# Performance work log

Measured on AMD Instinct MI355X. Metric: run time of the kernel, lower is better.

## Reference

```python
import jax, jax.numpy as jnp
import numpy as np

EMBED = 1024
HEADS = 16
HEAD_DIM = EMBED // HEADS
N, L = 8, 1024


def setup_inputs() -> dict:
    key = jax.random.key(0)
    ks = jax.random.split(key, 12)
    s = 1.0 / np.sqrt(EMBED)
    return {
        "values": jax.random.normal(ks[0], (N, L, EMBED), jnp.float32),
        "keys": jax.random.normal(ks[1], (N, L, EMBED), jnp.float32),
        "queries": jax.random.normal(ks[2], (N, L, EMBED), jnp.float32),
        "mask": jax.random.randint(ks[3], (N, 1, L, L), 0, 2, jnp.int32),
        "Wv": jax.random.normal(ks[4], (EMBED, EMBED), jnp.float32) * s,
        "bv": jnp.zeros((EMBED,), jnp.float32),
        "Wk": jax.random.normal(ks[5], (EMBED, EMBED), jnp.float32) * s,
        "bk": jnp.zeros((EMBED,), jnp.float32),
        "Wq": jax.random.normal(ks[6], (EMBED, EMBED), jnp.float32) * s,
        "bq": jnp.zeros((EMBED,), jnp.float32),
        "Wo": jax.random.normal(ks[7], (EMBED, EMBED), jnp.float32) * s,
        "bo": jnp.zeros((EMBED,), jnp.float32),
    }


def reference(values, keys, queries, mask, Wv, bv, Wk, bk, Wq, bq, Wo, bo):
    n, q_len = queries.shape[0], queries.shape[1]
    # Linear projections (torch Linear: x @ W.T + b)
    v = values @ Wv.T + bv
    k = keys @ Wk.T + bk
    q = queries @ Wq.T + bq
    # split heads: [N, L, H, D]
    v = v.reshape(n, -1, HEADS, HEAD_DIM)
    k = k.reshape(n, -1, HEADS, HEAD_DIM)
    q = q.reshape(n, q_len, HEADS, HEAD_DIM)
    # energy: [N, H, Q, K]
    energy = jnp.einsum("nqhd,nkhd->nhqk", q, k)
    energy = jnp.where(mask == 0, jnp.float32(-1e20), energy)
    attention = jax.nn.softmax(energy / jnp.sqrt(jnp.float32(EMBED)), axis=3)
    out = jnp.einsum("nhqk,nkhd->nqhd", attention, v).reshape(n, q_len, EMBED)
    return out @ Wo.T + bo
```

## Files before the change

kernel.cpp:

```cpp
#include <hip/hip_runtime.h>
#include <hip/hip_bf16.h>


typedef __attribute__((ext_vector_type(8))) short short8;
typedef __attribute__((ext_vector_type(8))) __bf16 bf16x8;
typedef __attribute__((ext_vector_type(4))) float f32x4;
typedef __attribute__((ext_vector_type(16))) float f32x16;

static __device__ __forceinline__ unsigned short f2bf(float x) {
  union { float f; unsigned u; } v; v.f = x;
  unsigned r = v.u + 0x7FFFu + ((v.u >> 16) & 1u);
  return (unsigned short)(r >> 16);
}

static __device__ __forceinline__ f32x4 mfma16(short8 a, short8 b, f32x4 c) {
  return __builtin_amdgcn_mfma_f32_16x16x32_bf16(
      __builtin_bit_cast(bf16x8, a), __builtin_bit_cast(bf16x8, b), c, 0, 0, 0);
}
static __device__ __forceinline__ f32x16 mfma32(short8 a, short8 b, f32x16 c) {
  return __builtin_amdgcn_mfma_f32_32x32x16_bf16(
      __builtin_bit_cast(bf16x8, a), __builtin_bit_cast(bf16x8, b), c, 0, 0, 0);
}

static __device__ __forceinline__ void gll16(const unsigned short* g, unsigned short* l) {
  __builtin_amdgcn_global_load_lds(
      (const __attribute__((address_space(1))) unsigned int*)(const void*)g,
      (__attribute__((address_space(3))) unsigned int*)(void*)l, 16, 0, 0);
}

static __device__ __forceinline__ unsigned cvtpk(float lo, float hi) {
  unsigned r;
  asm("v_cvt_pk_bf16_f32 %0, %1, %2" : "=v"(r) : "v"(lo), "v"(hi));
  return r;
}

static __device__ __forceinline__ void cvt8(const float* __restrict__ in,
                                            unsigned short* __restrict__ out, int i) {
  float4 a = ((const float4*)in)[i * 2];
  float4 b = ((const float4*)in)[i * 2 + 1];
  union { short8 v; unsigned short u[8]; } pk;
  pk.u[0] = f2bf(a.x); pk.u[1] = f2bf(a.y); pk.u[2] = f2bf(a.z); pk.u[3] = f2bf(a.w);
  pk.u[4] = f2bf(b.x); pk.u[5] = f2bf(b.y); pk.u[6] = f2bf(b.z); pk.u[7] = f2bf(b.w);
  ((short8*)out)[i] = pk.v;
}

__global__ __launch_bounds__(256)
void fused_pre(const float* __restrict__ queries, const float* __restrict__ keys,
               const float* __restrict__ values,
               const float* __restrict__ Wq, const float* __restrict__ Wk,
               const float* __restrict__ Wv, const float* __restrict__ Wo,
               const int* __restrict__ mask,
               unsigned short* __restrict__ Xq, unsigned short* __restrict__ Xk,
               unsigned short* __restrict__ Xv,
               unsigned short* __restrict__ W4, unsigned long long* __restrict__ M64)
{
  const int bid = blockIdx.x, tid = threadIdx.x;
  if (bid < 4096) {
    cvt8(queries, Xq, bid * 256 + tid);
  } else if (bid < 8192) {
    cvt8(keys, Xk, (bid - 4096) * 256 + tid);
  } else if (bid < 10240) {
    const int wsel = (bid - 8192) >> 9;
    const float* src = wsel == 0 ? Wq : wsel == 1 ? Wk : wsel == 2 ? Wv : Wo;
    cvt8(src, W4 + wsel * 1048576, ((bid - 8192) & 511) * 256 + tid);
  } else if (bid < 11264) {
    const int lane = tid & 63, wid = tid >> 6;
    const int gw = (bid - 10240) * 4 + wid;
#pragma unroll 4
    for (int j = 0; j < 32; ++j) {
      const int w = gw * 32 + j;
      unsigned long long b = __ballot(mask[(size_t)w * 64 + lane] != 0);
      if (lane == 0) M64[w] = b;
    }
  } else {
    cvt8(values, Xv, (bid - 11264) * 256 + tid);
  }
}

template<int MODE>
__global__ __launch_bounds__(256)
void gemm_kernel(const unsigned short* __restrict__ A, const unsigned short* __restrict__ B,
                 const float* __restrict__ bias, void* __restrict__ outp, float oscale)
{
  __shared__ alignas(16) unsigned short As[128][32];
  __shared__ alignas(16) unsigned short Bs[128][32];
  const int tid = threadIdx.x, lane = tid & 63, wid = tid >> 6;
  const int l15 = lane & 15, lg = lane >> 4;
  const int j = blockIdx.x >> 3;
  int bm, bn;
  if (MODE == 3) { bn = (blockIdx.x & 7) * 8 + (j & 7); bm = j >> 3; }
  else           { bm = (blockIdx.x & 7) * 8 + (j & 7); bn = j >> 3; }
  const int wr = (wid >> 1) * 64, wc = (wid & 1) * 64;

  f32x4 acc[4][4] = {};
  const int o = wid * 1024 + lane * 16;
  const unsigned short* gA0 = A + (size_t)(bm * 128 + (o >> 6)) * 1024 + ((o & 63) >> 1);
  const unsigned short* gA1 = gA0 + 64 * 1024;
  const unsigned short* gB0 = B + (size_t)(bn * 128 + (o >> 6)) * 1024 + ((o & 63) >> 1);
  const unsigned short* gB1 = gB0 + 64 * 1024;
  unsigned short* lA0 = &As[0][0] + wid * 512;
  unsigned short* lA1 = lA0 + 2048;
  unsigned short* lB0 = &Bs[0][0] + wid * 512;
  unsigned short* lB1 = lB0 + 2048;

  for (int k0 = 0; k0 < 1024; k0 += 32) {
    __syncthreads();
    gll16(gA0 + k0, lA0); gll16(gA1 + k0, lA1);
    gll16(gB0 + k0, lB0); gll16(gB1 + k0, lB1);
    __syncthreads();
    short8 af[4], bf[4];
#pragma unroll
    for (int f = 0; f < 4; ++f) {
      af[f] = *(const short8*)&As[wr + f * 16 + l15][lg * 8];
      bf[f] = *(const short8*)&Bs[wc + f * 16 + l15][lg * 8];
    }
#pragma unroll
    for (int r = 0; r < 4; ++r)
#pragma unroll
      for (int c = 0; c < 4; ++c)
        acc[r][c] = mfma16(af[r], bf[c], acc[r][c]);
  }

#pragma unroll
  for (int r = 0; r < 4; ++r) {
    const int mb = bm * 128 + wr + r * 16 + lg * 4;
#pragma unroll
    for (int c = 0; c < 4; ++c) {
      const int col = bn * 128 + wc + c * 16 + l15;
      if (MODE == 0) {
        const float bv = bias[col];
        unsigned short* O = (unsigned short*)outp;
#pragma unroll
        for (int i = 0; i < 4; ++i)
          O[(size_t)(mb + i) * 1024 + col] = f2bf((acc[r][c][i] + bv) * oscale);
      } else if (MODE == 3) {
        unsigned short* O = (unsigned short*)outp;
#pragma unroll
        for (int i = 0; i < 4; ++i)
          O[(size_t)(mb + i) * 8192 + col] = f2bf(acc[r][c][i] + bias[mb + i]);
      } else {
        const float bv = bias[col];
        float* O = (float*)outp;
#pragma unroll
        for (int i = 0; i < 4; ++i)
          O[(size_t)(mb + i) * 1024 + col] = acc[r][c][i] + bv;
      }
    }
  }
}

__global__ __launch_bounds__(256)
void attn_kernel(const unsigned short* __restrict__ Q,
                 const unsigned short* __restrict__ K,
                 const unsigned short* __restrict__ VT,
                 const unsigned long long* __restrict__ M64,
                 unsigned short* __restrict__ AO)
{
  __shared__ alignas(16) unsigned short KV[2][8192];
  const int tid = threadIdx.x, lane = tid & 63, wid = tid >> 6;
  const int l31 = lane & 31, hi = lane >> 5, hi4 = hi * 4;
  const int w = (blockIdx.x & 7) * 128 + (blockIdx.x >> 3);
  const int qt = w & 7, nh = w >> 3, h = nh & 15, n = nh >> 4;
  const int qbase = qt * 128 + wid * 32;

  const unsigned short* src[4];
  unsigned short* dst0[4];
  int tstride;
  if (wid < 2) {
#pragma unroll
    for (int i = 0; i < 4; ++i) {
      const int g = wid * 4 + i, c = g >> 1, kh = g & 1;
      src[i] = K + ((size_t)(n * 1024 + kh * 32 + l31) << 10) + h * 64 + c * 16 + hi * 8;
      dst0[i] = &KV[0][g * 512];
    }
    tstride = 64 * 1024;
  } else {
#pragma unroll
    for (int i = 0; i < 4; ++i) {
      const int g = (wid - 2) * 4 + i, kt = g >> 1, dh = g & 1;
      src[i] = VT + (size_t)(h * 64 + dh * 32 + l31) * 8192 + n * 1024 + kt * 16 + hi * 8;
      dst0[i] = &KV[0][4096 + g * 512];
    }
    tstride = 64;
  }

  short8 qf[4];
#pragma unroll
  for (int c = 0; c < 4; ++c)
    qf[c] = *(const short8*)&Q[(size_t)(n * 1024 + qbase + l31) * 1024 + h * 64 + c * 16 + hi * 8];

  const unsigned long long* Mq = M64 + (size_t)(n * 1024 + qbase + l31) * 16;
  unsigned long long mw = Mq[0], mwn = 0;

  f32x16 oacc0 = {}, oacc1 = {}, lacc = {};
  short8 ones;
#pragma unroll
  for (int j = 0; j < 8; ++j) ones[j] = (short)0x3F80;

#pragma unroll
  for (int i = 0; i < 4; ++i) gll16(src[i], dst0[i]);

  int cur = 0;
#pragma unroll 2
  for (int t = 0; t < 16; ++t) {
    __syncthreads();
    if (t < 15) {
      const size_t off = (size_t)(t + 1) * tstride;
#pragma unroll
      for (int i = 0; i < 4; ++i) gll16(src[i] + off, dst0[i] + (cur ^ 1) * 8192);
      mwn = Mq[t + 1];
    }
    const unsigned short* Kb = &KV[cur][0];

    f32x16 s0 = {}, s1 = {};
    __builtin_amdgcn_s_setprio(1);
#pragma unroll
    for (int c = 0; c < 4; ++c) {
      short8 kf0 = *(const short8*)&Kb[(c * 2 + 0) * 512 + lane * 8];
      short8 kf1 = *(const short8*)&Kb[(c * 2 + 1) * 512 + lane * 8];
      s0 = mfma32(kf0, qf[c], s0);
      s1 = mfma32(kf1, qf[c], s1);
    }
    __builtin_amdgcn_s_setprio(0);

    const unsigned wlo = (unsigned)mw >> hi4;
    const unsigned whi = (unsigned)(mw >> 32) >> hi4;
#pragma unroll
    for (int kt = 0; kt < 2; ++kt) {
      const unsigned wsh = kt ? whi : wlo;
      const f32x16& sv = kt ? s1 : s0;
      float p[16];
#pragma unroll
      for (int r = 0; r < 16; ++r) {
        const float pe = exp2f(sv[r]);
        const int pos = 8 * (r >> 2) + (r & 3);
        const int msk = ((int)(wsh << (31 - pos))) >> 31;
        p[r] = __builtin_bit_cast(float, __builtin_bit_cast(int, pe) & msk);
      }
      unsigned u[4][2];
#pragma unroll
      for (int g = 0; g < 4; ++g) {
        u[g][0] = cvtpk(p[4 * g], p[4 * g + 1]);
        u[g][1] = cvtpk(p[4 * g + 2], p[4 * g + 3]);
      }
      short8 pa0, pa1;
#pragma unroll
      for (int m = 0; m < 2; ++m) {
        unsigned a0 = u[2 * m][0], b0 = u[2 * m + 1][0];
        unsigned a1 = u[2 * m][1], b1 = u[2 * m + 1][1];
        asm("v_permlane32_swap_b32 %0, %1" : "+v"(a0), "+v"(b0));
        asm("v_permlane32_swap_b32 %0, %1" : "+v"(a1), "+v"(b1));
        union { unsigned uu[4]; short8 v; } pk;
        pk.uu[0] = a0; pk.uu[1] = a1; pk.uu[2] = b0; pk.uu[3] = b1;
        if (m == 0) pa0 = pk.v; else pa1 = pk.v;
      }
      __builtin_amdgcn_s_setprio(1);
      {
        const int g0 = (kt * 2 + 0) * 2, g1 = (kt * 2 + 1) * 2;
        short8 vf00 = *(const short8*)&Kb[4096 + (g0 + 0) * 512 + lane * 8];
        short8 vf01 = *(const short8*)&Kb[4096 + (g0 + 1) * 512 + lane * 8];
        short8 vf10 = *(const short8*)&Kb[4096 + (g1 + 0) * 512 + lane * 8];
        short8 vf11 = *(const short8*)&Kb[4096 + (g1 + 1) * 512 + lane * 8];
        oacc0 = mfma32(pa0, vf00, oacc0);
        oacc1 = mfma32(pa0, vf01, oacc1);
        lacc  = mfma32(pa0, ones, lacc);
        oacc0 = mfma32(pa1, vf10, oacc0);
        oacc1 = mfma32(pa1, vf11, oacc1);
        lacc  = mfma32(pa1, ones, lacc);
      }
      __builtin_amdgcn_s_setprio(0);
    }

    mw = mwn;
    cur ^= 1;
  }

#pragma unroll
  for (int r = 0; r < 16; ++r) {
    const int qrow = 8 * (r >> 2) + (r & 3) + hi4;
    const float rl = 1.0f / lacc[r];
    const size_t row = (size_t)(n * 1024 + qbase + qrow) * 1024 + h * 64;
    AO[row + l31]      = f2bf(oacc0[r] * rl);
    AO[row + 32 + l31] = f2bf(oacc1[r] * rl);
  }
}

extern "C" void kernel_launch(void* const* d_in, const int* in_sizes, int n_in,
                              void* d_out, int out_size, void* d_ws, size_t ws_size,
                              hipStream_t stream) {
  (void)in_sizes; (void)n_in; (void)out_size; (void)ws_size;
  const float* values  = (const float*)d_in[0];
  const float* keys    = (const float*)d_in[1];
  const float* queries = (const float*)d_in[2];
  const int*   mask    = (const int*)d_in[3];
  const float* Wv = (const float*)d_in[4];
  const float* bv = (const float*)d_in[5];
  const float* Wk = (const float*)d_in[6];
  const float* bk = (const float*)d_in[7];
  const float* Wq = (const float*)d_in[8];
  const float* bq = (const float*)d_in[9];
  const float* Wo = (const float*)d_in[10];
  const float* bo = (const float*)d_in[11];

  const size_t MB = 1u << 20;
  char* ws = (char*)d_ws;
  unsigned short* R0  = (unsigned short*)(ws);
  unsigned short* R16 = (unsigned short*)(ws + 16 * MB);
  unsigned short* Qb  = (unsigned short*)(ws + 32 * MB);
  unsigned short* Kb  = (unsigned short*)(ws + 48 * MB);
  unsigned short* W4  = (unsigned short*)(ws + 64 * MB);
  unsigned long long* M64 = (unsigned long long*)(ws + 72 * MB);
  unsigned short* Xv  = (unsigned short*)d_out;

  const dim3 b256(256);
  const float SCFULL = 0.03125f * 1.44269504089f;

  fused_pre<<<dim3(15360), b256, 0, stream>>>(
      queries, keys, values, Wq, Wk, Wv, Wo, mask, R0, R16, Xv, W4, M64);
  gemm_kernel<0><<<dim3(512), b256, 0, stream>>>(R0,  W4,           bq, (void*)Qb, SCFULL);
  gemm_kernel<0><<<dim3(512), b256, 0, stream>>>(R16, W4 + 1048576, bk, (void*)Kb, 1.0f);
  gemm_kernel<3><<<dim3(512), b256, 0, stream>>>(W4 + 2 * 1048576, Xv,
                                                 bv, (void*)R16, 1.0f);
  attn_kernel<<<dim3(1024), b256, 0, stream>>>(Qb, Kb, R16, M64, R0 );
  gemm_kernel<2><<<dim3(512), b256, 0, stream>>>(R0, W4 + 3 * 1048576, bo, d_out, 1.0f);
}
```

Baseline: 213.8 us.

## Double-buffer GEMM LDS tiles with BK=64 and XOR-swizzled layout

Rewrites the GEMM main loop to double-buffer the A/B shared-memory tiles. The next K-slice is prefetched while MFMAs run on the current one. The K step grows from 32 to 64, which halves the barriers per tile. An XOR swizzle on the LDS column chunks is meant to avoid bank conflicts on the fragment reads. The trade-offs are double the LDS footprint, which may lower occupancy, and a single barrier per iteration, which depends on the async global-to-LDS loads having completed before they are read.

```diff
diff --git a/kernel.cpp b/kernel.cpp
--- a/kernel.cpp
+++ b/kernel.cpp
@@ -82,8 +82,8 @@
 void gemm_kernel(const unsigned short* __restrict__ A, const unsigned short* __restrict__ B,
                  const float* __restrict__ bias, void* __restrict__ outp, float oscale)
 {
-  __shared__ alignas(16) unsigned short As[128][32];
-  __shared__ alignas(16) unsigned short Bs[128][32];
+  __shared__ alignas(16) unsigned short As[2][8192];
+  __shared__ alignas(16) unsigned short Bs[2][8192];
   const int tid = threadIdx.x, lane = tid & 63, wid = tid >> 6;
   const int l15 = lane & 15, lg = lane >> 4;
   const int j = blockIdx.x >> 3;
@@ -93,32 +93,56 @@
   const int wr = (wid >> 1) * 64, wc = (wid & 1) * 64;
 
   f32x4 acc[4][4] = {};
-  const int o = wid * 1024 + lane * 16;
-  const unsigned short* gA0 = A + (size_t)(bm * 128 + (o >> 6)) * 1024 + ((o & 63) >> 1);
-  const unsigned short* gA1 = gA0 + 64 * 1024;
-  const unsigned short* gB0 = B + (size_t)(bn * 128 + (o >> 6)) * 1024 + ((o & 63) >> 1);
-  const unsigned short* gB1 = gB0 + 64 * 1024;
-  unsigned short* lA0 = &As[0][0] + wid * 512;
-  unsigned short* lA1 = lA0 + 2048;
-  unsigned short* lB0 = &Bs[0][0] + wid * 512;
-  unsigned short* lB1 = lB0 + 2048;
-
-  for (int k0 = 0; k0 < 1024; k0 += 32) {
+
+  const unsigned short* gA[4];
+  const unsigned short* gB[4];
+  unsigned short* lA[4];
+  unsigned short* lB[4];
+#pragma unroll
+  for (int i = 0; i < 4; ++i) {
+    const int so = i * 2048 + tid * 8;
+    const int row = so >> 6;
+    const int ch = (so >> 3) & 7;
+    const int scol = (ch ^ (row & 7)) * 8;
+    gA[i] = A + (size_t)(bm * 128 + row) * 1024 + scol;
+    gB[i] = B + (size_t)(bn * 128 + row) * 1024 + scol;
+    lA[i] = &As[0][0] + so;
+    lB[i] = &Bs[0][0] + so;
+  }
+
+#pragma unroll
+  for (int i = 0; i < 4; ++i) { gll16(gA[i], lA[i]); gll16(gB[i], lB[i]); }
+
+  int cur = 0;
+#pragma unroll 2
+  for (int k0 = 0; k0 < 1024; k0 += 64) {
     __syncthreads();
-    gll16(gA0 + k0, lA0); gll16(gA1 + k0, lA1);
-    gll16(gB0 + k0, lB0); gll16(gB1 + k0, lB1);
-    __syncthreads();
-    short8 af[4], bf[4];
-#pragma unroll
-    for (int f = 0; f < 4; ++f) {
-      af[f] = *(const short8*)&As[wr + f * 16 + l15][lg * 8];
-      bf[f] = *(const short8*)&Bs[wc + f * 16 + l15][lg * 8];
-    }
-#pragma unroll
-    for (int r = 0; r < 4; ++r)
-#pragma unroll
-      for (int c = 0; c < 4; ++c)
-        acc[r][c] = mfma16(af[r], bf[c], acc[r][c]);
+    if (k0 + 64 < 1024) {
+      const int nb = (cur ^ 1) * 8192;
+#pragma unroll
+      for (int i = 0; i < 4; ++i) {
+        gll16(gA[i] + k0 + 64, lA[i] + nb);
+        gll16(gB[i] + k0 + 64, lB[i] + nb);
+      }
+    }
+    const unsigned short* Ab = &As[cur][0];
+    const unsigned short* Bb = &Bs[cur][0];
+#pragma unroll
+    for (int h = 0; h < 2; ++h) {
+      short8 af[4], bf[4];
+#pragma unroll
+      for (int f = 0; f < 4; ++f) {
+        const int ra = wr + f * 16 + l15, rb = wc + f * 16 + l15;
+        af[f] = *(const short8*)&Ab[ra * 64 + (((h * 4 + lg) ^ (ra & 7)) * 8)];
+        bf[f] = *(const short8*)&Bb[rb * 64 + (((h * 4 + lg) ^ (rb & 7)) * 8)];
+      }
+#pragma unroll
+      for (int r = 0; r < 4; ++r)
+#pragma unroll
+        for (int c = 0; c < 4; ++c)
+          acc[r][c] = mfma16(af[r], bf[c], acc[r][c]);
+    }
+    cur ^= 1;
   }
 
 #pragma unroll
```

New measurement: 212.9 us, median of 2. No clear change (-0.4%).
